# Kernel tuning notes

Hardware: AMD Instinct MI355X
Metric: run time of the kernel (lower is better)

The kernel has to match this reference:

```python
import jax, jax.numpy as jnp
import numpy as np

B, N, D = 4, 2048, 1024
WIN, K, ALPHA = 4, 8, 0.3


def setup_inputs() -> dict:
    key = jax.random.key(0)
    ks = jax.random.split(key, 16)
    s_d = 1.0 / np.sqrt(D)
    s_2d = 1.0 / np.sqrt(2 * D)
    inp = {
        'mu': jax.random.normal(ks[0], (B, N, D), jnp.float32),
        'pheromone': jax.random.uniform(ks[1], (B, N), jnp.float32),
        'Wq': jax.random.normal(ks[2], (D, D), jnp.float32) * s_d,
        'bq': jnp.zeros((D,), jnp.float32),
        'Wk': jax.random.normal(ks[3], (D, D), jnp.float32) * s_d,
        'bk': jnp.zeros((D,), jnp.float32),
        'Wv': jax.random.normal(ks[4], (D, D), jnp.float32) * s_d,
        'bv': jnp.zeros((D,), jnp.float32),
        'Wm1': jax.random.normal(ks[5], (2 * D, D), jnp.float32) * s_2d,
        'bm1': jnp.zeros((D,), jnp.float32),
        'Wm2': jax.random.normal(ks[6], (D, D), jnp.float32) * s_d,
        'bm2': jnp.zeros((D,), jnp.float32),
        'Wo': jax.random.normal(ks[7], (2 * D, D), jnp.float32) * s_2d,
        'bo': jnp.zeros((D,), jnp.float32),
    }
    return inp


def reference(mu, pheromone, Wq, bq, Wk, bk, Wv, bv, Wm1, bm1, Wm2, bm2, Wo, bo):
    # ---- local windowed gather-MLP ----
    padded = jnp.pad(mu, ((0, 0), (WIN, 0), (0, 0)))  # causal left-pad
    neighbors = jnp.stack([padded[:, WIN - w:WIN - w + N, :] for w in range(1, WIN + 1)], axis=2)
    self_exp = jnp.broadcast_to(mu[:, :, None, :], neighbors.shape)
    cat = jnp.concatenate([self_exp, neighbors], axis=-1)
    h = jax.nn.silu(cat @ Wm1 + bm1) @ Wm2 + bm2
    local_msgs = h.mean(axis=2)  # (B,N,D)

    # ---- causal top-k attention with pheromone bias ----
    q = mu @ Wq + bq
    k = mu @ Wk + bk
    v = mu @ Wv + bv
    scale = 1.0 / jnp.sqrt(jnp.asarray(D, mu.dtype))
    scores = jnp.einsum('bnd,bmd->bnm', q, k) * scale  # (B,N,N)
    scores = scores + ALPHA * pheromone[:, None, :]
    row = jnp.arange(N)
    causal = jnp.where(row[None, :] > row[:, None], -jnp.inf, 0.0).astype(mu.dtype)
    scores = scores + causal[None]
    # top-k sparsification (N > K): softmax over the k kept scores, zeros elsewhere
    vals, idx = jax.lax.top_k(scores, K)  # (B,N,K)
    probs = jax.nn.softmax(vals, axis=-1)
    bi = jnp.arange(B)[:, None, None]
    ni = jnp.arange(N)[None, :, None]
    attn = jnp.zeros_like(scores).at[bi, ni, idx].set(probs)
    global_msgs = jnp.einsum('bnm,bmd->bnd', attn, v)

    return jnp.concatenate([local_msgs, global_msgs], axis=-1) @ Wo + bo
```

## Files before the change

### kernel.cpp

```cpp
#include <hip/hip_runtime.h>
#include <hip/hip_bf16.h>
#include <math.h>

#define B_ 4
#define N_ 2048
#define D_ 1024
#define WIN_ 4
#define KTOP 8
#define ALPHA_ 0.3f
#define SCALE_ (1.0f/32.0f)
#define NCH 16
#define TROW 36
#define TPLANE (128 * TROW)
#define INV2048 0.00048828125f

typedef unsigned short ushortT;
typedef _Float16 halfT;
typedef __attribute__((ext_vector_type(8))) _Float16 half8v;
typedef __attribute__((ext_vector_type(4))) float f32x4;

__device__ inline ushortT h2u(halfT h){ union{halfT h; ushortT u;} x; x.h=h; return x.u; }
__device__ inline halfT  u2h(ushortT u){ union{halfT h; ushortT u;} x; x.u=u; return x.h; }
__device__ inline float  uh2f(ushortT u){ return (float)u2h(u); }

__global__ __launch_bounds__(256)
void split2_mu(const float* __restrict__ src, ushortT* __restrict__ Pa,
               ushortT* __restrict__ Pb)
{
    size_t base = ((size_t)blockIdx.x * 256 + threadIdx.x) * 4;
    float4 v = *reinterpret_cast<const float4*>(&src[base]);
    float vv[4] = {v.x, v.y, v.z, v.w};
    ushort4 pa, pb;
#pragma unroll
    for (int j = 0; j < 4; ++j) {
        float f = vv[j];
        halfT a = (halfT)f;  float r = f - (float)a;
        halfT b = (halfT)(r * 2048.0f);
        ((ushortT*)&pa)[j] = h2u(a); ((ushortT*)&pb)[j] = h2u(b);
    }
    *reinterpret_cast<ushort4*>(&Pa[base]) = pa;
    *reinterpret_cast<ushort4*>(&Pb[base]) = pb;
}

__global__ __launch_bounds__(256)
void transpose_f2h(const float* __restrict__ W, ushortT* __restrict__ Wt,
                   int K, int Nn)
{
    __shared__ float t[32][33];
    const int k0 = blockIdx.x * 32, n0 = blockIdx.y * 32;
    const int tx = threadIdx.x & 31, ty8 = threadIdx.x >> 5;
#pragma unroll
    for (int p = 0; p < 4; ++p) {
        int kk = p * 8 + ty8;
        t[kk][tx] = W[(size_t)(k0 + kk) * Nn + n0 + tx];
    }
    __syncthreads();
#pragma unroll
    for (int p = 0; p < 4; ++p) {
        int nn = p * 8 + ty8;
        Wt[(size_t)(n0 + nn) * K + k0 + tx] = h2u((halfT)t[tx][nn]);
    }
}

__global__ __launch_bounds__(256)
void transpose_split2(const float* __restrict__ W, ushortT* __restrict__ Pa,
                      ushortT* __restrict__ Pb, int K, int Nn)
{
    __shared__ float t[32][33];
    const int k0 = blockIdx.x * 32, n0 = blockIdx.y * 32;
    const int tx = threadIdx.x & 31, ty8 = threadIdx.x >> 5;
#pragma unroll
    for (int p = 0; p < 4; ++p) {
        int kk = p * 8 + ty8;
        t[kk][tx] = W[(size_t)(k0 + kk) * Nn + n0 + tx];
    }
    __syncthreads();
#pragma unroll
    for (int p = 0; p < 4; ++p) {
        int nn = p * 8 + ty8;
        float f = t[tx][nn];
        halfT a = (halfT)f;  float r = f - (float)a;
        halfT b = (halfT)(r * 2048.0f);
        size_t o = (size_t)(n0 + nn) * K + k0 + tx;
        Pa[o] = h2u(a); Pb[o] = h2u(b);
    }
}

template<int OUT_HALF>
__global__ __launch_bounds__(256)
void mfma_gemm_h(const ushortT* __restrict__ A, int lda,
                 const ushortT* __restrict__ Bt, int ldb,
                 const float* __restrict__ bias,
                 void* __restrict__ Cout, int ldc, int K)
{
    __shared__ ushortT AsL[128 * 72];
    __shared__ ushortT BsL[128 * 72];
    const int tid = threadIdx.x;
    const int m0 = blockIdx.y * 128;
    const int n0 = blockIdx.x * 128;
    const int w = tid >> 6, lane = tid & 63;
    const int wr = w >> 1, wc = w & 1;

    f32x4 acc[4][4];
#pragma unroll
    for (int mi = 0; mi < 4; ++mi)
#pragma unroll
        for (int ni = 0; ni < 4; ++ni) acc[mi][ni] = (f32x4){0.f, 0.f, 0.f, 0.f};

    for (int k0 = 0; k0 < K; k0 += 64) {
#pragma unroll
        for (int it = 0; it < 4; ++it) {
            int idx = tid + it * 256;
            int row = idx >> 3, c = idx & 7;
            int4 va = *reinterpret_cast<const int4*>(&A[(size_t)(m0 + row) * lda + k0 + c * 8]);
            *reinterpret_cast<int4*>(&AsL[row * 72 + c * 8]) = va;
            int4 vb = *reinterpret_cast<const int4*>(&Bt[(size_t)(n0 + row) * ldb + k0 + c * 8]);
            *reinterpret_cast<int4*>(&BsL[row * 72 + c * 8]) = vb;
        }
        __syncthreads();
#pragma unroll
        for (int kh = 0; kh < 2; ++kh) {
            const int ko = kh * 32 + (lane >> 4) * 8;
            const int rr = lane & 15;
            half8v af[4], bf[4];
#pragma unroll
            for (int mi = 0; mi < 4; ++mi)
                af[mi] = *reinterpret_cast<const half8v*>(&AsL[(wr * 64 + mi * 16 + rr) * 72 + ko]);
#pragma unroll
            for (int ni = 0; ni < 4; ++ni)
                bf[ni] = *reinterpret_cast<const half8v*>(&BsL[(wc * 64 + ni * 16 + rr) * 72 + ko]);
#pragma unroll
            for (int mi = 0; mi < 4; ++mi)
#pragma unroll
                for (int ni = 0; ni < 4; ++ni)
                    acc[mi][ni] = __builtin_amdgcn_mfma_f32_16x16x32_f16(
                        af[mi], bf[ni], acc[mi][ni], 0, 0, 0);
        }
        __syncthreads();
    }

    const int r4 = (lane >> 4) * 4, cl = lane & 15;
#pragma unroll
    for (int mi = 0; mi < 4; ++mi)
#pragma unroll
        for (int ni = 0; ni < 4; ++ni) {
            int row = m0 + wr * 64 + mi * 16 + r4;
            int col = n0 + wc * 64 + ni * 16 + cl;
            float bb = bias ? bias[col] : 0.f;
#pragma unroll
            for (int r = 0; r < 4; ++r) {
                float v = acc[mi][ni][r] + bb;
                if (OUT_HALF)
                    ((ushortT*)Cout)[(size_t)(row + r) * ldc + col] = h2u((halfT)v);
                else
                    ((float*)Cout)[(size_t)(row + r) * ldc + col] = v;
            }
        }
}

__global__ __launch_bounds__(256)
void silu_mean(const float* __restrict__ A, const float* __restrict__ Nb,
               ushortT* __restrict__ Sb)
{
    size_t idx4 = (size_t)blockIdx.x * blockDim.x + threadIdx.x;
    size_t base = idx4 << 2;
    int n = (int)((base >> 10) & (N_ - 1));
    float4 a = *reinterpret_cast<const float4*>(&A[base]);
    float sx = 0.f, sy = 0.f, sz = 0.f, sw = 0.f;
#pragma unroll
    for (int w = 1; w <= WIN_; ++w) {
        float xx = a.x, xy = a.y, xz = a.z, xw = a.w;
        if (n >= w) {
            const float4 nb = *reinterpret_cast<const float4*>(&Nb[base - (size_t)w * D_]);
            xx += nb.x; xy += nb.y; xz += nb.z; xw += nb.w;
        }
        sx += xx / (1.f + __expf(-xx));
        sy += xy / (1.f + __expf(-xy));
        sz += xz / (1.f + __expf(-xz));
        sw += xw / (1.f + __expf(-xw));
    }
    ushort4 o = {h2u((halfT)(sx * 0.25f)), h2u((halfT)(sy * 0.25f)),
                 h2u((halfT)(sz * 0.25f)), h2u((halfT)(sw * 0.25f))};
    *reinterpret_cast<ushort4*>(&Sb[base]) = o;
}

__device__ inline void topk_insert(float (&tv)[KTOP], int (&ti)[KTOP], float s, int m)
{
    if ((s > tv[KTOP-1]) || (s == tv[KTOP-1] && m < ti[KTOP-1])) {
        float cs = s; int ci = m;
#pragma unroll
        for (int q = 0; q < KTOP; ++q) {
            bool beats = (cs > tv[q]) || (cs == tv[q] && ci < ti[q]);
            if (beats) { float t0 = tv[q]; int t1 = ti[q];
                         tv[q] = cs; ti[q] = ci; cs = t0; ci = t1; }
        }
    }
}

#define SPLIT3H_COMPUTE(T4, wr, wc, lane, acc0, acc1)                           \
    {                                                                           \
        const int rr_ = (lane) & 15, ko_ = ((lane) >> 4) * 8;                   \
        half8v ba0_ = *reinterpret_cast<const half8v*>(                         \
            &T4[2 * TPLANE + ((wc) * 32 + rr_) * TROW + ko_]);                  \
        half8v ba1_ = *reinterpret_cast<const half8v*>(                         \
            &T4[2 * TPLANE + ((wc) * 32 + 16 + rr_) * TROW + ko_]);             \
        half8v bB0_ = *reinterpret_cast<const half8v*>(                         \
            &T4[3 * TPLANE + ((wc) * 32 + rr_) * TROW + ko_]);                  \
        half8v bB1_ = *reinterpret_cast<const half8v*>(                         \
            &T4[3 * TPLANE + ((wc) * 32 + 16 + rr_) * TROW + ko_]);             \
        _Pragma("unroll")                                                       \
        for (int mi_ = 0; mi_ < 4; ++mi_) {                                     \
            half8v aA_ = *reinterpret_cast<const half8v*>(                      \
                &T4[0 * TPLANE + ((wr) * 64 + mi_ * 16 + rr_) * TROW + ko_]);   \
            acc0[mi_][0] = __builtin_amdgcn_mfma_f32_16x16x32_f16(              \
                aA_, ba0_, acc0[mi_][0], 0, 0, 0);                              \
            acc0[mi_][1] = __builtin_amdgcn_mfma_f32_16x16x32_f16(              \
                aA_, ba1_, acc0[mi_][1], 0, 0, 0);                              \
            acc1[mi_][0] = __builtin_amdgcn_mfma_f32_16x16x32_f16(              \
                aA_, bB0_, acc1[mi_][0], 0, 0, 0);                              \
            acc1[mi_][1] = __builtin_amdgcn_mfma_f32_16x16x32_f16(              \
                aA_, bB1_, acc1[mi_][1], 0, 0, 0);                              \
        }                                                                       \
        _Pragma("unroll")                                                       \
        for (int mi_ = 0; mi_ < 4; ++mi_) {                                     \
            half8v aB_ = *reinterpret_cast<const half8v*>(                      \
                &T4[1 * TPLANE + ((wr) * 64 + mi_ * 16 + rr_) * TROW + ko_]);   \
            acc1[mi_][0] = __builtin_amdgcn_mfma_f32_16x16x32_f16(              \
                aB_, ba0_, acc1[mi_][0], 0, 0, 0);                              \
            acc1[mi_][1] = __builtin_amdgcn_mfma_f32_16x16x32_f16(              \
                aB_, ba1_, acc1[mi_][1], 0, 0, 0);                              \
        }                                                                       \
    }

__global__ __launch_bounds__(512, 4)
void gemm_split3h(const ushortT* __restrict__ A0, const ushortT* __restrict__ A1,
                  const ushortT* __restrict__ B0, const ushortT* __restrict__ B1,
                  const float* __restrict__ bias,
                  ushortT* __restrict__ Pa, ushortT* __restrict__ Pb)
{
    __shared__ ushortT T4[4 * TPLANE];

    int lin = blockIdx.y * 8 + blockIdx.x;
    lin = (lin & 7) * 64 + (lin >> 3);
    const int m0 = (lin >> 3) * 128;
    const int n0 = (lin & 7) * 128;

    const int tid = threadIdx.x;
    const int wid = tid >> 6, lane = tid & 63;
    const int wr = wid >> 2, wc = wid & 3;
    const int rowL = tid >> 2, cL = tid & 3;

    const size_t offA = (size_t)(m0 + rowL) * D_ + cL * 8;
    const size_t offB = (size_t)(n0 + rowL) * D_ + cL * 8;
    const int ldst = rowL * TROW + cL * 8;

    f32x4 acc0[4][2], acc1[4][2];
#pragma unroll
    for (int mi = 0; mi < 4; ++mi) {
        acc0[mi][0] = (f32x4){0,0,0,0}; acc0[mi][1] = (f32x4){0,0,0,0};
        acc1[mi][0] = (f32x4){0,0,0,0}; acc1[mi][1] = (f32x4){0,0,0,0};
    }

    int4 s0, s1, s2, s3;
    s0 = *reinterpret_cast<const int4*>(&A0[offA]);
    s1 = *reinterpret_cast<const int4*>(&A1[offA]);
    s2 = *reinterpret_cast<const int4*>(&B0[offB]);
    s3 = *reinterpret_cast<const int4*>(&B1[offB]);

    for (int ks = 0; ks < 32; ++ks) {
        __syncthreads();
        *reinterpret_cast<int4*>(&T4[0 * TPLANE + ldst]) = s0;
        *reinterpret_cast<int4*>(&T4[1 * TPLANE + ldst]) = s1;
        *reinterpret_cast<int4*>(&T4[2 * TPLANE + ldst]) = s2;
        *reinterpret_cast<int4*>(&T4[3 * TPLANE + ldst]) = s3;
        __syncthreads();
        if (ks < 31) {
            const int kk = (ks + 1) * 32;
            s0 = *reinterpret_cast<const int4*>(&A0[offA + kk]);
            s1 = *reinterpret_cast<const int4*>(&A1[offA + kk]);
            s2 = *reinterpret_cast<const int4*>(&B0[offB + kk]);
            s3 = *reinterpret_cast<const int4*>(&B1[offB + kk]);
        }
        SPLIT3H_COMPUTE(T4, wr, wc, lane, acc0, acc1)
    }

    const int r4 = (lane >> 4) * 4, cl = lane & 15;
#pragma unroll
    for (int mi = 0; mi < 4; ++mi)
#pragma unroll
        for (int ni = 0; ni < 2; ++ni) {
            int col = n0 + wc * 32 + ni * 16 + cl;
            float bb = bias[col];
#pragma unroll
            for (int r = 0; r < 4; ++r) {
                int row = m0 + wr * 64 + mi * 16 + r4 + r;
                float v = acc0[mi][ni][r] + INV2048 * acc1[mi][ni][r] + bb;
                halfT a = (halfT)v;  float r1 = v - (float)a;
                halfT b = (halfT)(r1 * 2048.0f);
                size_t o = (size_t)row * D_ + col;
                Pa[o] = h2u(a); Pb[o] = h2u(b);
            }
        }
}

__global__ __launch_bounds__(512, 4)
void attn_scores_h(const ushortT* __restrict__ Qa, const ushortT* __restrict__ QB,
                   const ushortT* __restrict__ Ka, const ushortT* __restrict__ KB,
                   const float* __restrict__ pher,
                   float* __restrict__ WV, int* __restrict__ WI)
{
    __shared__ ushortT T4[4 * TPLANE];
    __shared__ float Ps[128];
    __shared__ float PV[32 * 4 * 8];
    __shared__ int   PI[32 * 4 * 8];
    float* MV = reinterpret_cast<float*>(&T4[0]);
    int*   MI = reinterpret_cast<int*>((char*)&T4[0] + 16384);

    int lin = blockIdx.y * 136 + blockIdx.x;
    lin = (lin & 7) * 68 + (lin >> 3);
    const int b = lin / 136;
    const int xy = lin - b * 136;
    int g = 0;
    while ((g + 1) * (g + 2) / 2 <= xy) ++g;
    const int ch = xy - g * (g + 1) / 2;
    const int n0 = g * 128;
    const int m0 = ch * 128;
    const size_t bN = (size_t)b * N_;

    const int tid = threadIdx.x;
    const int wid = tid >> 6, lane = tid & 63;
    const int wr = wid >> 2, wc = wid & 3;
    const int rowL = tid >> 2, cL = tid & 3;

    if (tid < 128) Ps[tid] = pher[bN + m0 + tid];

    const size_t offQ = (bN + n0 + rowL) * (size_t)D_ + cL * 8;
    const size_t offK = (bN + m0 + rowL) * (size_t)D_ + cL * 8;
    const int ldst = rowL * TROW + cL * 8;

    f32x4 acc0[4][2], acc1[4][2];
#pragma unroll
    for (int mi = 0; mi < 4; ++mi) {
        acc0[mi][0] = (f32x4){0,0,0,0}; acc0[mi][1] = (f32x4){0,0,0,0};
        acc1[mi][0] = (f32x4){0,0,0,0}; acc1[mi][1] = (f32x4){0,0,0,0};
    }

    int4 s0, s1, s2, s3;
    s0 = *reinterpret_cast<const int4*>(&Qa[offQ]);
    s1 = *reinterpret_cast<const int4*>(&QB[offQ]);
    s2 = *reinterpret_cast<const int4*>(&Ka[offK]);
    s3 = *reinterpret_cast<const int4*>(&KB[offK]);

    for (int ks = 0; ks < 32; ++ks) {
        __syncthreads();
        *reinterpret_cast<int4*>(&T4[0 * TPLANE + ldst]) = s0;
        *reinterpret_cast<int4*>(&T4[1 * TPLANE + ldst]) = s1;
        *reinterpret_cast<int4*>(&T4[2 * TPLANE + ldst]) = s2;
        *reinterpret_cast<int4*>(&T4[3 * TPLANE + ldst]) = s3;
        __syncthreads();
        if (ks < 31) {
            const int kk = (ks + 1) * 32;
            s0 = *reinterpret_cast<const int4*>(&Qa[offQ + kk]);
            s1 = *reinterpret_cast<const int4*>(&QB[offQ + kk]);
            s2 = *reinterpret_cast<const int4*>(&Ka[offK + kk]);
            s3 = *reinterpret_cast<const int4*>(&KB[offK + kk]);
        }
        SPLIT3H_COMPUTE(T4, wr, wc, lane, acc0, acc1)
    }

    const int r4 = (lane >> 4) * 4, cl = lane & 15;
    for (int p = 0; p < 4; ++p) {
        __syncthreads();
        if (wr == (p >> 1)) {
#pragma unroll
            for (int mi2 = 0; mi2 < 2; ++mi2) {
                const int mi = (p & 1) * 2 + mi2;
#pragma unroll
                for (int ni = 0; ni < 2; ++ni) {
                    int col = wc * 32 + ni * 16 + cl;
                    int m = m0 + col;
#pragma unroll
                    for (int r = 0; r < 4; ++r) {
                        int rloc = mi2 * 16 + r4 + r;
                        int n = n0 + p * 32 + rloc;
                        bool ok = (m <= n);
                        float sc = acc0[mi][ni][r] + INV2048 * acc1[mi][ni][r];
                        MV[rloc * 128 + col] = ok ? (sc * SCALE_ + ALPHA_ * Ps[col])
                                                  : -INFINITY;
                        MI[rloc * 128 + col] = ok ? m : 0x7fffffff;
                    }
                }
            }
        }
        __syncthreads();
        if (tid < 128) {
            const int row = tid >> 2, q4 = tid & 3;
            float tv[KTOP]; int ti[KTOP];
#pragma unroll
            for (int j = 0; j < KTOP; ++j) { tv[j] = -INFINITY; ti[j] = 0x7fffffff; }
            for (int j = 0; j < 32; ++j) {
                float s2 = MV[row * 128 + q4 * 32 + j];
                if (s2 == -INFINITY) continue;
                topk_insert(tv, ti, s2, MI[row * 128 + q4 * 32 + j]);
            }
#pragma unroll
            for (int j = 0; j < KTOP; ++j) {
                PV[(row * 4 + q4) * 8 + j] = tv[j];
                PI[(row * 4 + q4) * 8 + j] = ti[j];
            }
        }
        __syncthreads();
        if (tid < 32) {
            float tv[KTOP]; int ti[KTOP];
#pragma unroll
            for (int j = 0; j < KTOP; ++j) { tv[j] = -INFINITY; ti[j] = 0x7fffffff; }
            for (int i = 0; i < 32; ++i) {
                float s2 = PV[tid * 32 + i];
                if (s2 == -INFINITY) continue;
                topk_insert(tv, ti, s2, PI[tid * 32 + i]);
            }
            int n = n0 + p * 32 + tid;
            size_t base = ((bN + n) * NCH + ch) * 8;
#pragma unroll
            for (int j = 0; j < KTOP; ++j) { WV[base + j] = tv[j]; WI[base + j] = ti[j]; }
        }
    }
}

__global__ __launch_bounds__(256)
void attn_merge(const float* __restrict__ WV, const int* __restrict__ WI,
                const ushortT* __restrict__ V, ushortT* __restrict__ CCb)
{
    __shared__ float CV[4][128];
    __shared__ int   CI[4][128];
    __shared__ float Pp[4][KTOP];
    __shared__ int   Pi[4][KTOP];

    const int tid  = threadIdx.x;
    const int wv   = tid >> 6;
    const int lane = tid & 63;
    const int rid  = blockIdx.x * 4 + wv;
    const int b    = rid >> 11;
    const int n    = rid & (N_ - 1);
    const int ncand = ((n >> 7) + 1) * 8;
    const size_t cbase = (size_t)rid * (NCH * 8);

#pragma unroll
    for (int t = 0; t < 2; ++t) {
        int i = lane + t * 64;
        if (i < ncand) { CV[wv][i] = WV[cbase + i]; CI[wv][i] = WI[cbase + i]; }
        else           { CV[wv][i] = -INFINITY;     CI[wv][i] = 0x7fffffff;   }
    }
    __syncthreads();

    if (lane == 0) {
        float tv[KTOP]; int ti[KTOP];
#pragma unroll
        for (int j = 0; j < KTOP; ++j) { tv[j] = -INFINITY; ti[j] = 0x7fffffff; }
        for (int i = 0; i < 128; ++i) {
            float s = CV[wv][i];
            if (s == -INFINITY) continue;
            topk_insert(tv, ti, s, CI[wv][i]);
        }
        float mx = tv[0];
        float e[KTOP]; float sum = 0.f;
#pragma unroll
        for (int j = 0; j < KTOP; ++j) {
            e[j] = (tv[j] == -INFINITY) ? 0.f : __expf(tv[j] - mx);
            sum += e[j];
        }
        float inv = 1.f / sum;
#pragma unroll
        for (int j = 0; j < KTOP; ++j) {
            Pp[wv][j] = e[j] * inv;
            Pi[wv][j] = (tv[j] == -INFINITY) ? 0 : ti[j];
        }
    }
    __syncthreads();

    const size_t vbase = (size_t)b * N_ * D_;
#pragma unroll
    for (int it = 0; it < 2; ++it) {
        int c8 = (it * 64 + lane) * 8;
        float o[8];
#pragma unroll
        for (int u = 0; u < 8; ++u) o[u] = 0.f;
#pragma unroll
        for (int j = 0; j < KTOP; ++j) {
            float p = Pp[wv][j];
            ushort4 v0 = *reinterpret_cast<const ushort4*>(
                &V[vbase + (size_t)Pi[wv][j] * D_ + c8]);
            ushort4 v1 = *reinterpret_cast<const ushort4*>(
                &V[vbase + (size_t)Pi[wv][j] * D_ + c8 + 4]);
            o[0] = fmaf(p, uh2f(v0.x), o[0]); o[1] = fmaf(p, uh2f(v0.y), o[1]);
            o[2] = fmaf(p, uh2f(v0.z), o[2]); o[3] = fmaf(p, uh2f(v0.w), o[3]);
            o[4] = fmaf(p, uh2f(v1.x), o[4]); o[5] = fmaf(p, uh2f(v1.y), o[5]);
            o[6] = fmaf(p, uh2f(v1.z), o[6]); o[7] = fmaf(p, uh2f(v1.w), o[7]);
        }
        ushort4 ob0 = {h2u((halfT)o[0]), h2u((halfT)o[1]), h2u((halfT)o[2]), h2u((halfT)o[3])};
        ushort4 ob1 = {h2u((halfT)o[4]), h2u((halfT)o[5]), h2u((halfT)o[6]), h2u((halfT)o[7])};
        *reinterpret_cast<ushort4*>(&CCb[(size_t)rid * 2048 + 1024 + c8]) = ob0;
        *reinterpret_cast<ushort4*>(&CCb[(size_t)rid * 2048 + 1024 + c8 + 4]) = ob1;
    }
}

extern "C" void kernel_launch(void* const* d_in, const int* in_sizes, int n_in,
                              void* d_out, int out_size, void* d_ws, size_t ws_size,
                              hipStream_t stream)
{
    const float* mu   = (const float*)d_in[0];
    const float* pher = (const float*)d_in[1];
    const float* Wq   = (const float*)d_in[2];
    const float* bq   = (const float*)d_in[3];
    const float* Wk   = (const float*)d_in[4];
    const float* bk   = (const float*)d_in[5];
    const float* Wv   = (const float*)d_in[6];
    const float* bv   = (const float*)d_in[7];
    const float* Wm1  = (const float*)d_in[8];
    const float* bm1  = (const float*)d_in[9];
    const float* Wm2  = (const float*)d_in[10];
    const float* bm2  = (const float*)d_in[11];
    const float* Wo   = (const float*)d_in[12];
    const float* bo   = (const float*)d_in[13];
    float* out = (float*)d_out;
    float* ws  = (float*)d_ws;

    const size_t SZ  = (size_t)B_ * N_ * D_;
    const size_t MEG = 1024 * 1024;
    const int M = B_ * N_;

    ushortT* CCb  = (ushortT*)ws;
    float*   AbF  = ws + SZ;
    float*   NbF  = ws + 2 * SZ;
    ushortT* Qa   = (ushortT*)(ws + SZ);
    ushortT* QB   = Qa + SZ;
    ushortT* Ka   = (ushortT*)(ws + 2 * SZ);
    ushortT* KB   = Ka + SZ;
    ushortT* mu_a = (ushortT*)(ws + 3 * SZ);
    ushortT* mu_B = mu_a + SZ;
    ushortT* Sb   = (ushortT*)(ws + 4 * SZ);
    float*   WVb  = (float*)(ws + 4 * SZ);
    int*     WIb  = (int*)(WVb + MEG);
    ushortT* Vb16 = (ushortT*)(ws + 4 * SZ + 2 * MEG);
    ushortT* U    = (ushortT*)(ws + 4 * SZ + 2 * MEG + SZ / 2);
    ushortT* Wt_m1 = U;
    ushortT* Wt_m2 = U + 2 * MEG;
    ushortT* Wt_v  = U + 3 * MEG;
    ushortT* WqT_a = U + 4 * MEG;        ushortT* WqT_B = U + 5 * MEG;
    ushortT* WkT_a = U + 6 * MEG;        ushortT* WkT_B = U + 7 * MEG;
    ushortT* Wt_o  = U + 8 * MEG;

    dim3 blk256(256), blk512(512);
    dim3 gD(8, 64);

    hipLaunchKernelGGL(split2_mu, dim3(SZ / 4 / 256), blk256, 0, stream, mu, mu_a, mu_B);
    hipLaunchKernelGGL(transpose_f2h, dim3(64, 32), blk256, 0, stream, Wm1, Wt_m1, 2048, 1024);
    hipLaunchKernelGGL(transpose_f2h, dim3(32, 32), blk256, 0, stream, Wm2, Wt_m2, 1024, 1024);
    hipLaunchKernelGGL(transpose_f2h, dim3(32, 32), blk256, 0, stream, Wv, Wt_v, 1024, 1024);
    hipLaunchKernelGGL(transpose_f2h, dim3(64, 32), blk256, 0, stream, Wo, Wt_o, 2048, 1024);
    hipLaunchKernelGGL(transpose_split2, dim3(32, 32), blk256, 0, stream,
                       Wq, WqT_a, WqT_B, 1024, 1024);
    hipLaunchKernelGGL(transpose_split2, dim3(32, 32), blk256, 0, stream,
                       Wk, WkT_a, WkT_B, 1024, 1024);
    hipLaunchKernelGGL((mfma_gemm_h<0>), gD, blk256, 0, stream,
                       mu_a, D_, Wt_m1, 2048, bm1, (void*)AbF, D_, D_);
    hipLaunchKernelGGL((mfma_gemm_h<0>), gD, blk256, 0, stream,
                       mu_a, D_, Wt_m1 + 1024, 2048, (const float*)nullptr, (void*)NbF, D_, D_);
    hipLaunchKernelGGL(silu_mean, dim3(SZ / 4 / 256), blk256, 0, stream, AbF, NbF, Sb);
    hipLaunchKernelGGL((mfma_gemm_h<1>), gD, blk256, 0, stream,
                       Sb, D_, Wt_m2, D_, bm2, (void*)CCb, 2 * D_, D_);
    hipLaunchKernelGGL((mfma_gemm_h<1>), gD, blk256, 0, stream,
                       mu_a, D_, Wt_v, D_, bv, (void*)Vb16, D_, D_);
    hipLaunchKernelGGL(gemm_split3h, gD, blk512, 0, stream,
                       mu_a, mu_B, WqT_a, WqT_B, bq, Qa, QB);
    hipLaunchKernelGGL(gemm_split3h, gD, blk512, 0, stream,
                       mu_a, mu_B, WkT_a, WkT_B, bk, Ka, KB);
    hipLaunchKernelGGL(attn_scores_h, dim3(136, B_), blk512, 0, stream,
                       Qa, QB, Ka, KB, pher, WVb, WIb);
    hipLaunchKernelGGL(attn_merge, dim3(M / 4), blk256, 0, stream, WVb, WIb, Vb16, CCb);
    hipLaunchKernelGGL((mfma_gemm_h<0>), gD, blk256, 0, stream,
                       CCb, 2 * D_, Wt_o, 2048, bo, (void*)out, D_, 2 * D_);

    (void)in_sizes; (void)n_in; (void)out_size; (void)ws_size;
}
```

Before: 774.3 us.

## Shrink split-fp16 GEMM and score tiles to 128x64 with 256-thread blocks

The split-precision Q/K GEMM and the causal score kernel now use 128x64 output tiles with 4 waves instead of 128x128 with 8 waves. This doubles the grid and the number of causal chunks per row, so the candidate buffers double and the merge kernel gains a two-level top-k reduction. The aim is better occupancy and load balance across CUs, traded against more re-reading of the A operand and a larger top-k merge.

```diff
diff --git a/kernel.cpp b/kernel.cpp
--- a/kernel.cpp
+++ b/kernel.cpp
@@ -9,10 +9,15 @@
 #define KTOP 8
 #define ALPHA_ 0.3f
 #define SCALE_ (1.0f/32.0f)
-#define NCH 16
+#define NCH2 32
 #define TROW 36
-#define TPLANE (128 * TROW)
 #define INV2048 0.00048828125f
+
+#define OFF_A0 0
+#define OFF_A1 (128 * TROW)
+#define OFF_B0 (2 * 128 * TROW)
+#define OFF_B1 (OFF_B0 + 64 * TROW)
+#define T4SZ   (OFF_B1 + 64 * TROW)
 
 typedef unsigned short ushortT;
 typedef _Float16 halfT;
@@ -197,21 +202,21 @@
     }
 }
 
-#define SPLIT3H_COMPUTE(T4, wr, wc, lane, acc0, acc1)                           \
+#define SPLIT3H_CORE(T4, wr, wc, lane, acc0, acc1)                              \
     {                                                                           \
         const int rr_ = (lane) & 15, ko_ = ((lane) >> 4) * 8;                   \
         half8v ba0_ = *reinterpret_cast<const half8v*>(                         \
-            &T4[2 * TPLANE + ((wc) * 32 + rr_) * TROW + ko_]);                  \
+            &T4[OFF_B0 + ((wc) * 32 + rr_) * TROW + ko_]);                      \
         half8v ba1_ = *reinterpret_cast<const half8v*>(                         \
-            &T4[2 * TPLANE + ((wc) * 32 + 16 + rr_) * TROW + ko_]);             \
+            &T4[OFF_B0 + ((wc) * 32 + 16 + rr_) * TROW + ko_]);                 \
         half8v bB0_ = *reinterpret_cast<const half8v*>(                         \
-            &T4[3 * TPLANE + ((wc) * 32 + rr_) * TROW + ko_]);                  \
+            &T4[OFF_B1 + ((wc) * 32 + rr_) * TROW + ko_]);                      \
         half8v bB1_ = *reinterpret_cast<const half8v*>(                         \
-            &T4[3 * TPLANE + ((wc) * 32 + 16 + rr_) * TROW + ko_]);             \
+            &T4[OFF_B1 + ((wc) * 32 + 16 + rr_) * TROW + ko_]);                 \
         _Pragma("unroll")                                                       \
         for (int mi_ = 0; mi_ < 4; ++mi_) {                                     \
             half8v aA_ = *reinterpret_cast<const half8v*>(                      \
-                &T4[0 * TPLANE + ((wr) * 64 + mi_ * 16 + rr_) * TROW + ko_]);   \
+                &T4[OFF_A0 + ((wr) * 64 + mi_ * 16 + rr_) * TROW + ko_]);       \
             acc0[mi_][0] = __builtin_amdgcn_mfma_f32_16x16x32_f16(              \
                 aA_, ba0_, acc0[mi_][0], 0, 0, 0);                              \
             acc0[mi_][1] = __builtin_amdgcn_mfma_f32_16x16x32_f16(              \
@@ -224,7 +229,7 @@
         _Pragma("unroll")                                                       \
         for (int mi_ = 0; mi_ < 4; ++mi_) {                                     \
             half8v aB_ = *reinterpret_cast<const half8v*>(                      \
-                &T4[1 * TPLANE + ((wr) * 64 + mi_ * 16 + rr_) * TROW + ko_]);   \
+                &T4[OFF_A1 + ((wr) * 64 + mi_ * 16 + rr_) * TROW + ko_]);       \
             acc1[mi_][0] = __builtin_amdgcn_mfma_f32_16x16x32_f16(              \
                 aB_, ba0_, acc1[mi_][0], 0, 0, 0);                              \
             acc1[mi_][1] = __builtin_amdgcn_mfma_f32_16x16x32_f16(              \
@@ -232,27 +237,50 @@
         }                                                                       \
     }
 
-__global__ __launch_bounds__(512, 4)
+#define S3H_LOAD(kk)                                                            \
+    {                                                                           \
+        sA0[0] = *reinterpret_cast<const int4*>(&PA0_[oQ0_ + (kk)]);            \
+        sA0[1] = *reinterpret_cast<const int4*>(&PA0_[oQ1_ + (kk)]);            \
+        sA1[0] = *reinterpret_cast<const int4*>(&PA1_[oQ0_ + (kk)]);            \
+        sA1[1] = *reinterpret_cast<const int4*>(&PA1_[oQ1_ + (kk)]);            \
+        sB0    = *reinterpret_cast<const int4*>(&PB0_[oK_ + (kk)]);             \
+        sB1    = *reinterpret_cast<const int4*>(&PB1_[oK_ + (kk)]);             \
+    }
+#define S3H_STORE()                                                             \
+    {                                                                           \
+        *reinterpret_cast<int4*>(&T4[OFF_A0 + ldstQ0]) = sA0[0];                \
+        *reinterpret_cast<int4*>(&T4[OFF_A0 + ldstQ1]) = sA0[1];                \
+        *reinterpret_cast<int4*>(&T4[OFF_A1 + ldstQ0]) = sA1[0];                \
+        *reinterpret_cast<int4*>(&T4[OFF_A1 + ldstQ1]) = sA1[1];                \
+        *reinterpret_cast<int4*>(&T4[OFF_B0 + ldstK]) = sB0;                    \
+        *reinterpret_cast<int4*>(&T4[OFF_B1 + ldstK]) = sB1;                    \
+    }
+
+__global__ __launch_bounds__(256, 4)
 void gemm_split3h(const ushortT* __restrict__ A0, const ushortT* __restrict__ A1,
                   const ushortT* __restrict__ B0, const ushortT* __restrict__ B1,
                   const float* __restrict__ bias,
                   ushortT* __restrict__ Pa, ushortT* __restrict__ Pb)
 {
-    __shared__ ushortT T4[4 * TPLANE];
-
-    int lin = blockIdx.y * 8 + blockIdx.x;
-    lin = (lin & 7) * 64 + (lin >> 3);
-    const int m0 = (lin >> 3) * 128;
-    const int n0 = (lin & 7) * 128;
+    __shared__ ushortT T4[T4SZ];
+
+    int lin = blockIdx.y * 16 + blockIdx.x;
+    lin = (lin & 7) * 128 + (lin >> 3);
+    const int m0 = (lin >> 4) * 128;
+    const int n0 = (lin & 15) * 64;
 
     const int tid = threadIdx.x;
     const int wid = tid >> 6, lane = tid & 63;
-    const int wr = wid >> 2, wc = wid & 3;
-    const int rowL = tid >> 2, cL = tid & 3;
-
-    const size_t offA = (size_t)(m0 + rowL) * D_ + cL * 8;
-    const size_t offB = (size_t)(n0 + rowL) * D_ + cL * 8;
-    const int ldst = rowL * TROW + cL * 8;
+    const int wr = wid >> 1, wc = wid & 1;
+    const int rowQ0 = tid >> 2, rowQ1 = (tid + 256) >> 2, cQ = tid & 3;
+
+    const ushortT *PA0_ = A0, *PA1_ = A1, *PB0_ = B0, *PB1_ = B1;
+    const size_t oQ0_ = (size_t)(m0 + rowQ0) * D_ + cQ * 8;
+    const size_t oQ1_ = (size_t)(m0 + rowQ1) * D_ + cQ * 8;
+    const size_t oK_  = (size_t)(n0 + rowQ0) * D_ + cQ * 8;
+    const int ldstQ0 = rowQ0 * TROW + cQ * 8;
+    const int ldstQ1 = rowQ1 * TROW + cQ * 8;
+    const int ldstK  = rowQ0 * TROW + cQ * 8;
 
     f32x4 acc0[4][2], acc1[4][2];
 #pragma unroll
@@ -261,27 +289,15 @@
         acc1[mi][0] = (f32x4){0,0,0,0}; acc1[mi][1] = (f32x4){0,0,0,0};
     }
 
-    int4 s0, s1, s2, s3;
-    s0 = *reinterpret_cast<const int4*>(&A0[offA]);
-    s1 = *reinterpret_cast<const int4*>(&A1[offA]);
-    s2 = *reinterpret_cast<const int4*>(&B0[offB]);
-    s3 = *reinterpret_cast<const int4*>(&B1[offB]);
+    int4 sA0[2], sA1[2], sB0, sB1;
+    S3H_LOAD(0)
 
     for (int ks = 0; ks < 32; ++ks) {
         __syncthreads();
-        *reinterpret_cast<int4*>(&T4[0 * TPLANE + ldst]) = s0;
-        *reinterpret_cast<int4*>(&T4[1 * TPLANE + ldst]) = s1;
-        *reinterpret_cast<int4*>(&T4[2 * TPLANE + ldst]) = s2;
-        *reinterpret_cast<int4*>(&T4[3 * TPLANE + ldst]) = s3;
-        __syncthreads();
-        if (ks < 31) {
-            const int kk = (ks + 1) * 32;
-            s0 = *reinterpret_cast<const int4*>(&A0[offA + kk]);
-            s1 = *reinterpret_cast<const int4*>(&A1[offA + kk]);
-            s2 = *reinterpret_cast<const int4*>(&B0[offB + kk]);
-            s3 = *reinterpret_cast<const int4*>(&B1[offB + kk]);
-        }
-        SPLIT3H_COMPUTE(T4, wr, wc, lane, acc0, acc1)
+        S3H_STORE()
+        __syncthreads();
+        if (ks < 31) S3H_LOAD((ks + 1) * 32)
+        SPLIT3H_CORE(T4, wr, wc, lane, acc0, acc1)
     }
 
     const int r4 = (lane >> 4) * 4, cl = lane & 15;
@@ -303,40 +319,44 @@
         }
 }
 
-__global__ __launch_bounds__(512, 4)
+__global__ __launch_bounds__(256, 4)
 void attn_scores_h(const ushortT* __restrict__ Qa, const ushortT* __restrict__ QB,
                    const ushortT* __restrict__ Ka, const ushortT* __restrict__ KB,
                    const float* __restrict__ pher,
                    float* __restrict__ WV, int* __restrict__ WI)
 {
-    __shared__ ushortT T4[4 * TPLANE];
-    __shared__ float Ps[128];
-    __shared__ float PV[32 * 4 * 8];
-    __shared__ int   PI[32 * 4 * 8];
+    __shared__ ushortT T4[T4SZ];
+    __shared__ float Ps[64];
+    __shared__ float PV[32 * 2 * 8];
+    __shared__ int   PI[32 * 2 * 8];
     float* MV = reinterpret_cast<float*>(&T4[0]);
-    int*   MI = reinterpret_cast<int*>((char*)&T4[0] + 16384);
-
-    int lin = blockIdx.y * 136 + blockIdx.x;
-    lin = (lin & 7) * 68 + (lin >> 3);
-    const int b = lin / 136;
-    const int xy = lin - b * 136;
+    int*   MI = reinterpret_cast<int*>((char*)&T4[0] + 8192);
+
+    int lin = blockIdx.y * 272 + blockIdx.x;
+    lin = (lin & 7) * 136 + (lin >> 3);
+    const int b = lin / 272;
+    const int xy = lin - b * 272;
     int g = 0;
-    while ((g + 1) * (g + 2) / 2 <= xy) ++g;
-    const int ch = xy - g * (g + 1) / 2;
+    while ((g + 1) * (g + 2) <= xy) ++g;
+    const int ch = xy - g * (g + 1);
     const int n0 = g * 128;
-    const int m0 = ch * 128;
+    const int m0 = ch * 64;
     const size_t bN = (size_t)b * N_;
 
     const int tid = threadIdx.x;
     const int wid = tid >> 6, lane = tid & 63;
-    const int wr = wid >> 2, wc = wid & 3;
-    const int rowL = tid >> 2, cL = tid & 3;
-
-    if (tid < 128) Ps[tid] = pher[bN + m0 + tid];
-
-    const size_t offQ = (bN + n0 + rowL) * (size_t)D_ + cL * 8;
-    const size_t offK = (bN + m0 + rowL) * (size_t)D_ + cL * 8;
-    const int ldst = rowL * TROW + cL * 8;
+    const int wr = wid >> 1, wc = wid & 1;
+    const int rowQ0 = tid >> 2, rowQ1 = (tid + 256) >> 2, cQ = tid & 3;
+
+    if (tid < 64) Ps[tid] = pher[bN + m0 + tid];
+
+    const ushortT *PA0_ = Qa, *PA1_ = QB, *PB0_ = Ka, *PB1_ = KB;
+    const size_t oQ0_ = (bN + n0 + rowQ0) * (size_t)D_ + cQ * 8;
+    const size_t oQ1_ = (bN + n0 + rowQ1) * (size_t)D_ + cQ * 8;
+    const size_t oK_  = (bN + m0 + rowQ0) * (size_t)D_ + cQ * 8;
+    const int ldstQ0 = rowQ0 * TROW + cQ * 8;
+    const int ldstQ1 = rowQ1 * TROW + cQ * 8;
+    const int ldstK  = rowQ0 * TROW + cQ * 8;
 
     f32x4 acc0[4][2], acc1[4][2];
 #pragma unroll
@@ -345,27 +365,15 @@
         acc1[mi][0] = (f32x4){0,0,0,0}; acc1[mi][1] = (f32x4){0,0,0,0};
     }
 
-    int4 s0, s1, s2, s3;
-    s0 = *reinterpret_cast<const int4*>(&Qa[offQ]);
-    s1 = *reinterpret_cast<const int4*>(&QB[offQ]);
-    s2 = *reinterpret_cast<const int4*>(&Ka[offK]);
-    s3 = *reinterpret_cast<const int4*>(&KB[offK]);
+    int4 sA0[2], sA1[2], sB0, sB1;
+    S3H_LOAD(0)
 
     for (int ks = 0; ks < 32; ++ks) {
         __syncthreads();
-        *reinterpret_cast<int4*>(&T4[0 * TPLANE + ldst]) = s0;
-        *reinterpret_cast<int4*>(&T4[1 * TPLANE + ldst]) = s1;
-        *reinterpret_cast<int4*>(&T4[2 * TPLANE + ldst]) = s2;
-        *reinterpret_cast<int4*>(&T4[3 * TPLANE + ldst]) = s3;
-        __syncthreads();
-        if (ks < 31) {
-            const int kk = (ks + 1) * 32;
-            s0 = *reinterpret_cast<const int4*>(&Qa[offQ + kk]);
-            s1 = *reinterpret_cast<const int4*>(&QB[offQ + kk]);
-            s2 = *reinterpret_cast<const int4*>(&Ka[offK + kk]);
-            s3 = *reinterpret_cast<const int4*>(&KB[offK + kk]);
-        }
-        SPLIT3H_COMPUTE(T4, wr, wc, lane, acc0, acc1)
+        S3H_STORE()
+        __syncthreads();
+        if (ks < 31) S3H_LOAD((ks + 1) * 32)
+        SPLIT3H_CORE(T4, wr, wc, lane, acc0, acc1)
     }
 
     const int r4 = (lane >> 4) * 4, cl = lane & 15;
@@ -385,28 +393,28 @@
                         int n = n0 + p * 32 + rloc;
                         bool ok = (m <= n);
                         float sc = acc0[mi][ni][r] + INV2048 * acc1[mi][ni][r];
-                        MV[rloc * 128 + col] = ok ? (sc * SCALE_ + ALPHA_ * Ps[col])
-                                                  : -INFINITY;
-                        MI[rloc * 128 + col] = ok ? m : 0x7fffffff;
+                        MV[rloc * 64 + col] = ok ? (sc * SCALE_ + ALPHA_ * Ps[col])
+                                                 : -INFINITY;
+                        MI[rloc * 64 + col] = ok ? m : 0x7fffffff;
                     }
                 }
             }
         }
         __syncthreads();
-        if (tid < 128) {
-            const int row = tid >> 2, q4 = tid & 3;
+        if (tid < 64) {
+            const int row = tid >> 1, q2 = tid & 1;
             float tv[KTOP]; int ti[KTOP];
 #pragma unroll
             for (int j = 0; j < KTOP; ++j) { tv[j] = -INFINITY; ti[j] = 0x7fffffff; }
             for (int j = 0; j < 32; ++j) {
-                float s2 = MV[row * 128 + q4 * 32 + j];
+                float s2 = MV[row * 64 + q2 * 32 + j];
                 if (s2 == -INFINITY) continue;
-                topk_insert(tv, ti, s2, MI[row * 128 + q4 * 32 + j]);
+                topk_insert(tv, ti, s2, MI[row * 64 + q2 * 32 + j]);
             }
 #pragma unroll
             for (int j = 0; j < KTOP; ++j) {
-                PV[(row * 4 + q4) * 8 + j] = tv[j];
-                PI[(row * 4 + q4) * 8 + j] = ti[j];
+                PV[(row * 2 + q2) * 8 + j] = tv[j];
+                PI[(row * 2 + q2) * 8 + j] = ti[j];
             }
         }
         __syncthreads();
@@ -414,13 +422,13 @@
             float tv[KTOP]; int ti[KTOP];
 #pragma unroll
             for (int j = 0; j < KTOP; ++j) { tv[j] = -INFINITY; ti[j] = 0x7fffffff; }
-            for (int i = 0; i < 32; ++i) {
-                float s2 = PV[tid * 32 + i];
+            for (int i = 0; i < 16; ++i) {
+                float s2 = PV[tid * 16 + i];
                 if (s2 == -INFINITY) continue;
-                topk_insert(tv, ti, s2, PI[tid * 32 + i]);
+                topk_insert(tv, ti, s2, PI[tid * 16 + i]);
             }
             int n = n0 + p * 32 + tid;
-            size_t base = ((bN + n) * NCH + ch) * 8;
+            size_t base = ((bN + n) * NCH2 + ch) * 8;
 #pragma unroll
             for (int j = 0; j < KTOP; ++j) { WV[base + j] = tv[j]; WI[base + j] = ti[j]; }
         }
@@ -431,8 +439,10 @@
 void attn_merge(const float* __restrict__ WV, const int* __restrict__ WI,
                 const ushortT* __restrict__ V, ushortT* __restrict__ CCb)
 {
-    __shared__ float CV[4][128];
-    __shared__ int   CI[4][128];
+    __shared__ float CV[4][256];
+    __shared__ int   CI[4][256];
+    __shared__ float PP[4][4][KTOP];
+    __shared__ int   II[4][4][KTOP];
     __shared__ float Pp[4][KTOP];
     __shared__ int   Pi[4][KTOP];
 
@@ -442,25 +452,39 @@
     const int rid  = blockIdx.x * 4 + wv;
     const int b    = rid >> 11;
     const int n    = rid & (N_ - 1);
-    const int ncand = ((n >> 7) + 1) * 8;
-    const size_t cbase = (size_t)rid * (NCH * 8);
-
-#pragma unroll
-    for (int t = 0; t < 2; ++t) {
+    const int ncand = ((n >> 6) + 1) * 8;
+    const size_t cbase = (size_t)rid * (NCH2 * 8);
+
+#pragma unroll
+    for (int t = 0; t < 4; ++t) {
         int i = lane + t * 64;
         if (i < ncand) { CV[wv][i] = WV[cbase + i]; CI[wv][i] = WI[cbase + i]; }
         else           { CV[wv][i] = -INFINITY;     CI[wv][i] = 0x7fffffff;   }
     }
     __syncthreads();
 
+    if (lane < 4) {
+        float tv[KTOP]; int ti[KTOP];
+#pragma unroll
+        for (int j = 0; j < KTOP; ++j) { tv[j] = -INFINITY; ti[j] = 0x7fffffff; }
+        for (int i = 0; i < 64; ++i) {
+            float s = CV[wv][lane * 64 + i];
+            if (s == -INFINITY) continue;
+            topk_insert(tv, ti, s, CI[wv][lane * 64 + i]);
+        }
+#pragma unroll
+        for (int j = 0; j < KTOP; ++j) { PP[wv][lane][j] = tv[j]; II[wv][lane][j] = ti[j]; }
+    }
+    __syncthreads();
+
     if (lane == 0) {
         float tv[KTOP]; int ti[KTOP];
 #pragma unroll
         for (int j = 0; j < KTOP; ++j) { tv[j] = -INFINITY; ti[j] = 0x7fffffff; }
-        for (int i = 0; i < 128; ++i) {
-            float s = CV[wv][i];
+        for (int i = 0; i < 32; ++i) {
+            float s = PP[wv][i >> 3][i & 7];
             if (s == -INFINITY) continue;
-            topk_insert(tv, ti, s, CI[wv][i]);
+            topk_insert(tv, ti, s, II[wv][i >> 3][i & 7]);
         }
         float mx = tv[0];
         float e[KTOP]; float sum = 0.f;
@@ -538,9 +562,9 @@
     ushortT* KB   = Ka + SZ;
     ushortT* mu_a = (ushortT*)(ws + 3 * SZ);
     ushortT* mu_B = mu_a + SZ;
+    float*   WVb  = (float*)(ws + 3 * SZ);
+    int*     WIb  = (int*)(WVb + 2 * MEG);
     ushortT* Sb   = (ushortT*)(ws + 4 * SZ);
-    float*   WVb  = (float*)(ws + 4 * SZ);
-    int*     WIb  = (int*)(WVb + MEG);
     ushortT* Vb16 = (ushortT*)(ws + 4 * SZ + 2 * MEG);
     ushortT* U    = (ushortT*)(ws + 4 * SZ + 2 * MEG + SZ / 2);
     ushortT* Wt_m1 = U;
@@ -550,7 +574,7 @@
     ushortT* WkT_a = U + 6 * MEG;        ushortT* WkT_B = U + 7 * MEG;
     ushortT* Wt_o  = U + 8 * MEG;
 
-    dim3 blk256(256), blk512(512);
+    dim3 blk256(256);
     dim3 gD(8, 64);
 
     hipLaunchKernelGGL(split2_mu, dim3(SZ / 4 / 256), blk256, 0, stream, mu, mu_a, mu_B);
@@ -571,11 +595,11 @@
                        Sb, D_, Wt_m2, D_, bm2, (void*)CCb, 2 * D_, D_);
     hipLaunchKernelGGL((mfma_gemm_h<1>), gD, blk256, 0, stream,
                        mu_a, D_, Wt_v, D_, bv, (void*)Vb16, D_, D_);
-    hipLaunchKernelGGL(gemm_split3h, gD, blk512, 0, stream,
+    hipLaunchKernelGGL(gemm_split3h, dim3(16, 64), blk256, 0, stream,
                        mu_a, mu_B, WqT_a, WqT_B, bq, Qa, QB);
-    hipLaunchKernelGGL(gemm_split3h, gD, blk512, 0, stream,
+    hipLaunchKernelGGL(gemm_split3h, dim3(16, 64), blk256, 0, stream,
                        mu_a, mu_B, WkT_a, WkT_B, bk, Ka, KB);
-    hipLaunchKernelGGL(attn_scores_h, dim3(136, B_), blk512, 0, stream,
+    hipLaunchKernelGGL(attn_scores_h, dim3(272, B_), blk256, 0, stream,
                        Qa, QB, Ka, KB, pher, WVb, WIb);
     hipLaunchKernelGGL(attn_merge, dim3(M / 4), blk256, 0, stream, WVb, WIb, Vb16, CCb);
     hipLaunchKernelGGL((mfma_gemm_h<0>), gD, blk256, 0, stream,
```

Result: slower. 1.182 ms (+52.7%).
